# Kernel tuning notes

Measured on AMD Instinct MI355X. Metric: run time of the kernel, lower is better.

Reference implementation:

```python
import math
import jax, jax.numpy as jnp
import numpy as np

DN = ('NCHW', 'OIHW', 'NCHW')

def _conv2d(x, w, b, stride, padding='VALID'):
    y = jax.lax.conv_general_dilated(x, w, window_strides=stride, padding=padding,
                                     dimension_numbers=DN)
    return y + b[None, :, None, None]

def _same_padding_conv(x, w, b, s):
    # replicate torch same_padding_conv: ceil-mode SAME padding, then VALID conv
    H, W = x.shape[2], x.shape[3]
    kh, kw = w.shape[2], w.shape[3]
    out_h, out_w = math.ceil(H / s[0]), math.ceil(W / s[1])
    pad_h = max((out_h - 1) * s[0] + kh - H, 0)
    pad_w = max((out_w - 1) * s[1] + kw - W, 0)
    pt, pl = pad_h // 2, pad_w // 2
    x = jnp.pad(x, ((0, 0), (0, 0), (pt, pad_h - pt), (pl, pad_w - pl)))
    return _conv2d(x, w, b, s)

def _leaky(x):
    return jax.nn.leaky_relu(x, negative_slope=0.2)

def setup_inputs() -> dict:
    key = jax.random.key(0)
    ks = jax.random.split(key, 8)
    B, cin, cout, H, W = 2, 16, 24, 384, 1280
    fl = jax.random.normal(ks[0], (B, cin, H, W), jnp.float32)
    fr = jax.random.normal(ks[1], (B, cin, H, W), jnp.float32)
    w_em = jax.random.normal(ks[2], (cout, cin, 4, 4), jnp.float32) * 0.05
    b_em = jax.random.normal(ks[3], (cout,), jnp.float32) * 0.05
    w_rc = jax.random.normal(ks[4], (cout, cout, 1, 1), jnp.float32) * 0.1
    b_rc = jax.random.normal(ks[5], (cout,), jnp.float32) * 0.05
    w_tf = jax.random.normal(ks[6], (13, cout + 1, 1, 1), jnp.float32) * 0.1
    b_tf = jax.random.normal(ks[7], (13,), jnp.float32) * 0.05
    return {'feature_left': fl, 'feature_right': fr, 'max_disp': 64,
            'w_em': w_em, 'b_em': b_em, 'w_rc': w_rc, 'b_rc': b_rc,
            'w_tf': w_tf, 'b_tf': b_tf}

def reference(feature_left, feature_right, max_disp, w_em, b_em, w_rc, b_rc, w_tf, b_tf):
    # left branch: 4x4 conv, stride (4,4), VALID (torch default padding=0)
    fl = _leaky(_conv2d(_leaky(_conv2d(feature_left, w_em, b_em, (4, 4))), w_rc, b_rc, (1, 1)))
    # right branch: same-padding conv with stride (4,1) -> full width retained
    fr = _leaky(_conv2d(_leaky(_same_padding_conv(feature_right, w_em, b_em, (4, 1))), w_rc, b_rc, (1, 1)))
    B, C, Hq, Wq = fl.shape
    Wr = fr.shape[3]
    # clipped gather indices: idx[d, x] = clip(4*x - d + 1, 0, Wr-1)
    d = jnp.arange(max_disp)[:, None]          # [D,1]
    x = jnp.arange(Wq)[None, :]                # [1,Wq]
    idx = jnp.clip(4 * x - d + 1, 0, Wr - 1)   # [D,Wq]
    fr_g = jnp.take(fr, idx, axis=3)           # [B,C,H,D,Wq]
    # L1 cost over channels -> [B,D,H,Wq]
    cost_volume = jnp.sum(jnp.abs(fl[:, :, :, None, :] - fr_g), axis=1).transpose(0, 2, 1, 3)
    cost_f = jnp.min(cost_volume, axis=1, keepdims=True)                  # [B,1,H,Wq]
    d_init = jnp.argmin(cost_volume, axis=1, keepdims=True).astype(fl.dtype)
    p_init = jnp.concatenate([cost_f, fl], axis=1)
    p_init = _leaky(_conv2d(p_init, w_tf, b_tf, (1, 1)))                  # [B,13,H,Wq]
    z = jnp.zeros_like(d_init)
    out = jnp.concatenate([d_init, z, z, p_init], axis=1)                 # [B,16,H,Wq]
    return out, cost_volume
```

## Files before the change

### kernel.cpp

```cpp
#include <hip/hip_runtime.h>

#define B_   2
#define CIN  16
#define HIN  384
#define WIN  1280
#define CO   24
#define HQ   96
#define WL   320
#define WR   1280
#define DMAX 64

__device__ __forceinline__ float lk(float v) { return v >= 0.f ? v : 0.2f * v; }

__global__ __launch_bounds__(256) void k_left(
    const float* __restrict__ x, const float* __restrict__ w_em,
    const float* __restrict__ b_em, const float* __restrict__ w_rc,
    const float* __restrict__ b_rc, float* __restrict__ out)
{
    __shared__ float smem[CO * CIN * 16];
    __shared__ float swt[CO * CO];
    __shared__ float sbe[CO], sbr[CO];

    for (int i = threadIdx.x; i < CO * CIN * 16; i += 256) smem[i] = w_em[i];
    for (int i = threadIdx.x; i < CO * CO; i += 256) swt[i] = w_rc[(i % CO) * CO + (i / CO)];
    if (threadIdx.x < CO) { sbe[threadIdx.x] = b_em[threadIdx.x]; sbr[threadIdx.x] = b_rc[threadIdx.x]; }
    __syncthreads();

    const int t = threadIdx.x;
    const int half = t >> 7, pxl = t & 127;
    const int obase = half * 12;
    const int flat = blockIdx.x * 128 + pxl;
    const int j = flat % WL, h = (flat / WL) % HQ, b = flat / (WL * HQ);

    float acc[12];
#pragma unroll
    for (int oo = 0; oo < 12; ++oo) acc[oo] = sbe[obase + oo];

    for (int c = 0; c < CIN; ++c) {
#pragma unroll
        for (int kh = 0; kh < 4; ++kh) {
            const float4 v = *(const float4*)(x + ((size_t)(b * CIN + c) * HIN + 4 * h + kh) * WIN + 4 * j);
#pragma unroll
            for (int oo = 0; oo < 12; ++oo) {
                const float4 wv = *(const float4*)&smem[(((obase + oo) * CIN + c) * 4 + kh) * 4];
                acc[oo] += v.x * wv.x + v.y * wv.y + v.z * wv.z + v.w * wv.w;
            }
        }
    }
    __syncthreads();
#pragma unroll
    for (int oo = 0; oo < 12; ++oo) smem[(obase + oo) * 128 + pxl] = lk(acc[oo]);
    __syncthreads();

    float acc2[12];
#pragma unroll
    for (int oo = 0; oo < 12; ++oo) acc2[oo] = sbr[obase + oo];
    for (int c = 0; c < CO; ++c) {
        const float in_c = smem[c * 128 + pxl];
#pragma unroll
        for (int oo = 0; oo < 12; ++oo) acc2[oo] += in_c * swt[c * CO + obase + oo];
    }
#pragma unroll
    for (int oo = 0; oo < 12; ++oo)
        out[((size_t)(b * CO + obase + oo) * HQ + h) * WL + j] = lk(acc2[oo]);
}

__global__ __launch_bounds__(256) void k_right(
    const float* __restrict__ x, const float* __restrict__ w_em,
    const float* __restrict__ b_em, const float* __restrict__ w_rc,
    const float* __restrict__ b_rc, float* __restrict__ out)
{
    __shared__ float smem[CO * CIN * 16];
    __shared__ float swt[CO * CO];
    __shared__ float sbe[CO], sbr[CO];

    for (int i = threadIdx.x; i < CO * CIN * 16; i += 256) smem[i] = w_em[i];
    for (int i = threadIdx.x; i < CO * CO; i += 256) swt[i] = w_rc[(i % CO) * CO + (i / CO)];
    if (threadIdx.x < CO) { sbe[threadIdx.x] = b_em[threadIdx.x]; sbr[threadIdx.x] = b_rc[threadIdx.x]; }
    __syncthreads();

    const int t = threadIdx.x;
    const int L = t & 63, quarter = t >> 6;
    const int obase = quarter * 6;
    const int row = blockIdx.x / 5, jbase = (blockIdx.x % 5) * 256;
    const int b = row / HQ, h = row % HQ;

    const bool vm1 = (jbase + 4 * L - 1) >= 0;
    const bool vp4 = (jbase + 4 * L + 4) < WIN;
    const bool vp5 = (jbase + 4 * L + 5) < WIN;
    const int  im1 = 4 * L - 1;
    const int  ip4 = 4 * L + 4;
    const int  ip5 = 4 * L + 5;

    float acc[4][6];
#pragma unroll
    for (int k = 0; k < 4; ++k)
#pragma unroll
        for (int oo = 0; oo < 6; ++oo) acc[k][oo] = sbe[obase + oo];

    for (int c = 0; c < CIN; ++c) {
#pragma unroll
        for (int kh = 0; kh < 4; ++kh) {
            const float* xr = x + ((size_t)(b * CIN + c) * HIN + 4 * h + kh) * WIN + jbase;
            const float4 v = *(const float4*)(xr + 4 * L);
            float in[7];
            in[0] = vm1 ? xr[im1] : 0.f;
            in[1] = v.x; in[2] = v.y; in[3] = v.z; in[4] = v.w;
            in[5] = vp4 ? xr[ip4] : 0.f;
            in[6] = vp5 ? xr[ip5] : 0.f;
#pragma unroll
            for (int oo = 0; oo < 6; ++oo) {
                const float4 wv = *(const float4*)&smem[(((obase + oo) * CIN + c) * 4 + kh) * 4];
#pragma unroll
                for (int k = 0; k < 4; ++k)
                    acc[k][oo] += in[k] * wv.x + in[k + 1] * wv.y + in[k + 2] * wv.z + in[k + 3] * wv.w;
            }
        }
    }
    __syncthreads();
#pragma unroll
    for (int oo = 0; oo < 6; ++oo) {
        float4 st = make_float4(lk(acc[0][oo]), lk(acc[1][oo]), lk(acc[2][oo]), lk(acc[3][oo]));
        *(float4*)&smem[(obase + oo) * 256 + 4 * L] = st;
    }
    __syncthreads();

    float acc2[CO];
#pragma unroll
    for (int o = 0; o < CO; ++o) acc2[o] = sbr[o];
    for (int c = 0; c < CO; ++c) {
        const float in_c = smem[c * 256 + t];
#pragma unroll
        for (int o = 0; o < CO; ++o) acc2[o] += in_c * swt[c * CO + o];
    }
#pragma unroll
    for (int o = 0; o < CO; ++o)
        out[((size_t)(b * CO + o) * HQ + h) * WR + jbase + t] = lk(acc2[o]);
}

__global__ __launch_bounds__(256) void k_cost(
    const float* __restrict__ fl, const float* __restrict__ fr,
    const float* __restrict__ wtf, const float* __restrict__ btf,
    float* __restrict__ out, float* __restrict__ cost)
{
    __shared__ float frs[4 * 12 * 81];
    __shared__ float sbest[256];
    __shared__ int   sbd[256];

    const int t  = threadIdx.x;
    const int j  = t & 63;
    const int dq = t >> 6;
    const int jc = blockIdx.x % 5;
    const int r  = blockIdx.x / 5;
    const int h  = r % HQ, b = r / HQ;
    const int j0 = jc * 64;
    const int jg = j0 + j;
    const int colbase = 4 * j0 - 64;

    float acc[16];
#pragma unroll
    for (int dl = 0; dl < 16; ++dl) acc[dl] = 0.f;

    for (int ch = 0; ch < 2; ++ch) {
        const int c0 = ch * 12;
        __syncthreads();
        for (int idx = t; idx < 12 * 320; idx += 256) {
            const int c = idx / 320, cp = idx % 320;
            const int col = colbase + cp;
            const float v = fr[((size_t)(b * CO + c0 + c) * HQ + h) * WR + (col > 0 ? col : 0)];
            frs[((cp & 3) * 12 + c) * 81 + (cp >> 2)] = v;
        }
        __syncthreads();

        for (int c = 0; c < 12; ++c) {
            const float flc = fl[((size_t)(b * CO + c0 + c) * HQ + h) * WL + jg];
#pragma unroll
            for (int p = 0; p < 4; ++p) {
                const int dp0 = (1 - p) & 3;
                const int q0 = j - 4 * dq + ((65 - dp0) >> 2);
                const int abase = (p * 12 + c) * 81 + q0;
#pragma unroll
                for (int i = 0; i < 4; ++i)
                    acc[dp0 + 4 * i] += fabsf(flc - frs[abase - i]);
            }
        }
    }

    const size_t cb0 = ((size_t)(b * DMAX + 16 * dq) * HQ + h) * WL + jg;
#pragma unroll
    for (int dl = 0; dl < 16; ++dl)
        cost[cb0 + (size_t)dl * (HQ * WL)] = acc[dl];

    float best = acc[0]; int bdl = 0;
#pragma unroll
    for (int dl = 1; dl < 16; ++dl)
        if (acc[dl] < best) { best = acc[dl]; bdl = dl; }
    sbest[t] = best; sbd[t] = 16 * dq + bdl;
    __syncthreads();

    if (t < 64) {
        float cur = sbest[j]; int curd = sbd[j];
#pragma unroll
        for (int g = 1; g < 4; ++g) {
            const float v = sbest[g * 64 + j];
            if (v < cur) { cur = v; curd = sbd[g * 64 + j]; }
        }
        float flr[CO];
#pragma unroll
        for (int c = 0; c < CO; ++c) flr[c] = fl[((size_t)(b * CO + c) * HQ + h) * WL + jg];
#pragma unroll
        for (int o = 0; o < 13; ++o) {
            float a = btf[o] + wtf[o * 25] * cur;
#pragma unroll
            for (int c = 0; c < CO; ++c) a += wtf[o * 25 + 1 + c] * flr[c];
            out[((size_t)(b * 16 + 3 + o) * HQ + h) * WL + jg] = lk(a);
        }
        out[((size_t)(b * 16 + 0) * HQ + h) * WL + jg] = (float)curd;
        out[((size_t)(b * 16 + 1) * HQ + h) * WL + jg] = 0.f;
        out[((size_t)(b * 16 + 2) * HQ + h) * WL + jg] = 0.f;
    }
}

extern "C" void kernel_launch(void* const* d_in, const int* in_sizes, int n_in,
                              void* d_out, int out_size, void* d_ws, size_t ws_size,
                              hipStream_t stream) {
    const float* fl_in = (const float*)d_in[0];
    const float* fr_in = (const float*)d_in[1];
    const float* w_em = (const float*)d_in[3];
    const float* b_em = (const float*)d_in[4];
    const float* w_rc = (const float*)d_in[5];
    const float* b_rc = (const float*)d_in[6];
    const float* w_tf = (const float*)d_in[7];
    const float* b_tf = (const float*)d_in[8];

    float* out  = (float*)d_out;
    float* cost = out + (size_t)B_ * 16 * HQ * WL;

    float* fl_ws = (float*)d_ws;
    float* fr_ws = fl_ws + (size_t)B_ * CO * HQ * WL;

    hipLaunchKernelGGL(k_left,  dim3(480), dim3(256), 0, stream,
                       fl_in, w_em, b_em, w_rc, b_rc, fl_ws);
    hipLaunchKernelGGL(k_right, dim3(960), dim3(256), 0, stream,
                       fr_in, w_em, b_em, w_rc, b_rc, fr_ws);
    hipLaunchKernelGGL(k_cost,  dim3(960), dim3(256), 0, stream,
                       fl_ws, fr_ws, w_tf, b_tf, out, cost);
}
```

Before: 269.3 us.

## Stage all channels of right features once and vectorize cost-volume LDS reads

The cost kernel now stages all 24 channels of the right-feature row into shared memory in one pass, in a plain linear layout with a small offset, instead of two passes of 12 channels in a 4-way phase-split layout. Each thread then reads four disparities per float4 LDS load. This cuts barrier pairs and scalar shared-memory reads. In exchange it uses more shared memory per block, which could lower occupancy. The right-branch conv also fetches its halo pixels as two float2 loads with clamped offsets, and uses a separate shared buffer for intermediate activations so one __syncthreads can be dropped. The launch order of the left and right kernels is swapped.

```diff
diff --git a/kernel.cpp b/kernel.cpp
--- a/kernel.cpp
+++ b/kernel.cpp
@@ -70,11 +70,12 @@
     const float* __restrict__ b_em, const float* __restrict__ w_rc,
     const float* __restrict__ b_rc, float* __restrict__ out)
 {
-    __shared__ float smem[CO * CIN * 16];
+    __shared__ float sw[CO * CIN * 16];
+    __shared__ float em[CO * 256];
     __shared__ float swt[CO * CO];
     __shared__ float sbe[CO], sbr[CO];
 
-    for (int i = threadIdx.x; i < CO * CIN * 16; i += 256) smem[i] = w_em[i];
+    for (int i = threadIdx.x; i < CO * CIN * 16; i += 256) sw[i] = w_em[i];
     for (int i = threadIdx.x; i < CO * CO; i += 256) swt[i] = w_rc[(i % CO) * CO + (i / CO)];
     if (threadIdx.x < CO) { sbe[threadIdx.x] = b_em[threadIdx.x]; sbr[threadIdx.x] = b_rc[threadIdx.x]; }
     __syncthreads();
@@ -85,12 +86,10 @@
     const int row = blockIdx.x / 5, jbase = (blockIdx.x % 5) * 256;
     const int b = row / HQ, h = row % HQ;
 
-    const bool vm1 = (jbase + 4 * L - 1) >= 0;
-    const bool vp4 = (jbase + 4 * L + 4) < WIN;
-    const bool vp5 = (jbase + 4 * L + 5) < WIN;
-    const int  im1 = 4 * L - 1;
-    const int  ip4 = 4 * L + 4;
-    const int  ip5 = 4 * L + 5;
+    const bool vm1 = (jbase + 4 * L) > 0;
+    const bool vp  = (jbase + 4 * L + 4) < WIN;
+    const int  om1 = vm1 ? (4 * L - 2) : 0;
+    const int  op4 = vp  ? (4 * L + 4) : 0;
 
     float acc[4][6];
 #pragma unroll
@@ -102,26 +101,27 @@
 #pragma unroll
         for (int kh = 0; kh < 4; ++kh) {
             const float* xr = x + ((size_t)(b * CIN + c) * HIN + 4 * h + kh) * WIN + jbase;
-            const float4 v = *(const float4*)(xr + 4 * L);
+            const float4  v = *(const float4*)(xr + 4 * L);
+            const float2  A = *(const float2*)(xr + om1);
+            const float2  C = *(const float2*)(xr + op4);
             float in[7];
-            in[0] = vm1 ? xr[im1] : 0.f;
+            in[0] = vm1 ? A.y : 0.f;
             in[1] = v.x; in[2] = v.y; in[3] = v.z; in[4] = v.w;
-            in[5] = vp4 ? xr[ip4] : 0.f;
-            in[6] = vp5 ? xr[ip5] : 0.f;
+            in[5] = vp ? C.x : 0.f;
+            in[6] = vp ? C.y : 0.f;
 #pragma unroll
             for (int oo = 0; oo < 6; ++oo) {
-                const float4 wv = *(const float4*)&smem[(((obase + oo) * CIN + c) * 4 + kh) * 4];
+                const float4 wv = *(const float4*)&sw[(((obase + oo) * CIN + c) * 4 + kh) * 4];
 #pragma unroll
                 for (int k = 0; k < 4; ++k)
                     acc[k][oo] += in[k] * wv.x + in[k + 1] * wv.y + in[k + 2] * wv.z + in[k + 3] * wv.w;
             }
         }
     }
-    __syncthreads();
 #pragma unroll
     for (int oo = 0; oo < 6; ++oo) {
         float4 st = make_float4(lk(acc[0][oo]), lk(acc[1][oo]), lk(acc[2][oo]), lk(acc[3][oo]));
-        *(float4*)&smem[(obase + oo) * 256 + 4 * L] = st;
+        *(float4*)&em[(obase + oo) * 256 + 4 * L] = st;
     }
     __syncthreads();
 
@@ -129,7 +129,7 @@
 #pragma unroll
     for (int o = 0; o < CO; ++o) acc2[o] = sbr[o];
     for (int c = 0; c < CO; ++c) {
-        const float in_c = smem[c * 256 + t];
+        const float in_c = em[c * 256 + t];
 #pragma unroll
         for (int o = 0; o < CO; ++o) acc2[o] += in_c * swt[c * CO + o];
     }
@@ -143,13 +143,13 @@
     const float* __restrict__ wtf, const float* __restrict__ btf,
     float* __restrict__ out, float* __restrict__ cost)
 {
-    __shared__ float frs[4 * 12 * 81];
+    __shared__ float frs[CO * 324];
     __shared__ float sbest[256];
     __shared__ int   sbd[256];
 
     const int t  = threadIdx.x;
     const int j  = t & 63;
-    const int dq = t >> 6;
+    const int w  = t >> 6;
     const int jc = blockIdx.x % 5;
     const int r  = blockIdx.x / 5;
     const int h  = r % HQ, b = r / HQ;
@@ -157,45 +157,51 @@
     const int jg = j0 + j;
     const int colbase = 4 * j0 - 64;
 
-    float acc[16];
-#pragma unroll
-    for (int dl = 0; dl < 16; ++dl) acc[dl] = 0.f;
-
-    for (int ch = 0; ch < 2; ++ch) {
-        const int c0 = ch * 12;
-        __syncthreads();
-        for (int idx = t; idx < 12 * 320; idx += 256) {
-            const int c = idx / 320, cp = idx % 320;
-            const int col = colbase + cp;
-            const float v = fr[((size_t)(b * CO + c0 + c) * HQ + h) * WR + (col > 0 ? col : 0)];
-            frs[((cp & 3) * 12 + c) * 81 + (cp >> 2)] = v;
-        }
-        __syncthreads();
-
-        for (int c = 0; c < 12; ++c) {
-            const float flc = fl[((size_t)(b * CO + c0 + c) * HQ + h) * WL + jg];
-#pragma unroll
-            for (int p = 0; p < 4; ++p) {
-                const int dp0 = (1 - p) & 3;
-                const int q0 = j - 4 * dq + ((65 - dp0) >> 2);
-                const int abase = (p * 12 + c) * 81 + q0;
-#pragma unroll
-                for (int i = 0; i < 4; ++i)
-                    acc[dp0 + 4 * i] += fabsf(flc - frs[abase - i]);
-            }
-        }
-    }
-
-    const size_t cb0 = ((size_t)(b * DMAX + 16 * dq) * HQ + h) * WL + jg;
-#pragma unroll
-    for (int dl = 0; dl < 16; ++dl)
-        cost[cb0 + (size_t)dl * (HQ * WL)] = acc[dl];
-
-    float best = acc[0]; int bdl = 0;
-#pragma unroll
-    for (int dl = 1; dl < 16; ++dl)
-        if (acc[dl] < best) { best = acc[dl]; bdl = dl; }
-    sbest[t] = best; sbd[t] = 16 * dq + bdl;
+    for (int idx = t; idx < CO * 320; idx += 256) {
+        const int c = idx / 320, Wd = idx % 320;
+        const int col = colbase + Wd;
+        frs[c * 324 + 2 + Wd] = fr[((size_t)(b * CO + c) * HQ + h) * WR + (col > 0 ? col : 0)];
+    }
+    __syncthreads();
+
+    float acc[4][4];
+#pragma unroll
+    for (int q = 0; q < 4; ++q)
+#pragma unroll
+        for (int rr = 0; rr < 4; ++rr) acc[q][rr] = 0.f;
+
+    for (int c = 0; c < CO; ++c) {
+        const float flc = fl[((size_t)(b * CO + c) * HQ + h) * WL + jg];
+        const float* base = &frs[c * 324 + 4 * j + 64];
+#pragma unroll
+        for (int q = 0; q < 4; ++q) {
+            const int D = 4 * w + q;
+            const float4 v = *(const float4*)(base - 4 * D);
+            acc[q][0] += fabsf(flc - v.w);
+            acc[q][1] += fabsf(flc - v.z);
+            acc[q][2] += fabsf(flc - v.y);
+            acc[q][3] += fabsf(flc - v.x);
+        }
+    }
+
+#pragma unroll
+    for (int q = 0; q < 4; ++q)
+#pragma unroll
+        for (int rr = 0; rr < 4; ++rr) {
+            const int d = 16 * w + 4 * q + rr;
+            cost[((size_t)(b * DMAX + d) * HQ + h) * WL + jg] = acc[q][rr];
+        }
+
+    float best = acc[0][0]; int bd = 16 * w;
+#pragma unroll
+    for (int q = 0; q < 4; ++q)
+#pragma unroll
+        for (int rr = 0; rr < 4; ++rr) {
+            if (q == 0 && rr == 0) continue;
+            const int d = 16 * w + 4 * q + rr;
+            if (acc[q][rr] < best) { best = acc[q][rr]; bd = d; }
+        }
+    sbest[t] = best; sbd[t] = bd;
     __syncthreads();
 
     if (t < 64) {
@@ -239,10 +245,10 @@
     float* fl_ws = (float*)d_ws;
     float* fr_ws = fl_ws + (size_t)B_ * CO * HQ * WL;
 
+    hipLaunchKernelGGL(k_right, dim3(960), dim3(256), 0, stream,
+                       fr_in, w_em, b_em, w_rc, b_rc, fr_ws);
     hipLaunchKernelGGL(k_left,  dim3(480), dim3(256), 0, stream,
                        fl_in, w_em, b_em, w_rc, b_rc, fl_ws);
-    hipLaunchKernelGGL(k_right, dim3(960), dim3(256), 0, stream,
-                       fr_in, w_em, b_em, w_rc, b_rc, fr_ws);
     hipLaunchKernelGGL(k_cost,  dim3(960), dim3(256), 0, stream,
                        fl_ws, fr_ws, w_tf, b_tf, out, cost);
 }
```

Result: faster. 250.0 us (-7.2%).
